# Performance work log

Measured on AMD Instinct MI355X. Metric: run time of the kernel, lower is better.

Reference implementation:

```python
import jax, jax.numpy as jnp
import numpy as np

B = 256          # graphs per batch
N_PER_G = 64     # nodes per graph
E_PER_G = 1024   # edges per graph
FN, FE, FG = 128, 128, 64
NA, HA, SO = 8, 256, 128


def _w(key, shape, scale=0.05):
    return jax.random.normal(key, shape, dtype=jnp.float32) * scale


def setup_inputs() -> dict:
    key = jax.random.key(0)
    ks = jax.random.split(key, 24)
    TN, TE = B * N_PER_G, B * E_PER_G
    inp = {
        'nodes': jax.random.normal(ks[0], (TN, FN), dtype=jnp.float32),
        'edges': jax.random.normal(ks[1], (TE, FE), dtype=jnp.float32),
        'globals_': jax.random.normal(ks[2], (B, FG), dtype=jnp.float32),
        'node_graph': jnp.repeat(jnp.arange(B, dtype=jnp.int32), N_PER_G),
        'edge_graph': jnp.repeat(jnp.arange(B, dtype=jnp.int32), E_PER_G),
        'a': jax.random.normal(ks[3], (B, NA), dtype=jnp.float32),
        # edge1: EdgeLinear(256, edge_features=FE)
        'We1': _w(ks[4], (FE, 256)), 'be1': jnp.zeros((256,), jnp.float32),
        # node1: NodeLinear(256, node_features=FN)
        'Wn1': _w(ks[5], (FN, 256)), 'bn1': jnp.zeros((256,), jnp.float32),
        # edge2: EdgeLinear(128, edge_features=256, global_features=FG)
        'We2_e': _w(ks[6], (256, 128)), 'We2_g': _w(ks[7], (FG, 128)), 'be2': jnp.zeros((128,), jnp.float32),
        # node2: NodeLinear(128, node_features=256, global_features=FG)
        'Wn2_n': _w(ks[8], (256, 128)), 'Wn2_g': _w(ks[9], (FG, 128)), 'bn2': jnp.zeros((128,), jnp.float32),
        # global: GlobalLinear(SO, node_features=128, edge_features=128, global_features=FG, aggregation='avg')
        'Wg_n': _w(ks[10], (128, SO)), 'Wg_e': _w(ks[11], (128, SO)), 'Wg_g': _w(ks[12], (FG, SO)), 'bg': jnp.zeros((SO,), jnp.float32),
        # action MLP
        'Wh': _w(ks[13], (SO + NA, HA)), 'bh': jnp.zeros((HA,), jnp.float32),
        'Wo': _w(ks[14], (HA, 1)), 'bo': jnp.zeros((1,), jnp.float32),
    }
    return inp


def _seg_mean(x, seg, num_segments):
    s = jax.ops.segment_sum(x, seg, num_segments=num_segments)
    c = jax.ops.segment_sum(jnp.ones((x.shape[0],), x.dtype), seg, num_segments=num_segments)
    return s / jnp.maximum(c, 1.0)[:, None]


def reference(nodes, edges, globals_, node_graph, edge_graph, a,
              We1, be1, Wn1, bn1, We2_e, We2_g, be2, Wn2_n, Wn2_g, bn2,
              Wg_n, Wg_e, Wg_g, bg, Wh, bh, Wo, bo):
    nb = globals_.shape[0]
    # edge1 + relu
    e = jax.nn.relu(edges @ We1 + be1)                                  # [TE,256]
    # node1 + relu
    n = jax.nn.relu(nodes @ Wn1 + bn1)                                  # [TN,256]
    # edge2 (edge feats + global broadcast to edges) + relu
    e = jax.nn.relu(e @ We2_e + globals_[edge_graph] @ We2_g + be2)     # [TE,128]
    # node2 (node feats + global broadcast to nodes) + relu
    n = jax.nn.relu(n @ Wn2_n + globals_[node_graph] @ Wn2_g + bn2)     # [TN,128]
    # global: avg-aggregate nodes and edges per graph + global linear
    n_avg = _seg_mean(n, node_graph, nb)                                # [B,128]
    e_avg = _seg_mean(e, edge_graph, nb)                                # [B,128]
    state_value = n_avg @ Wg_n + e_avg @ Wg_e + globals_ @ Wg_g + bg    # [B,SO]
    # action MLP
    sa = jnp.concatenate((state_value, a), axis=1)                      # [B,SO+NA]
    h = jax.nn.relu(sa @ Wh + bh)                                       # [B,HA]
    return h @ Wo + bo                                                  # [B,1]
```

## Files before the change

### kernel.cpp

```cpp
#include <hip/hip_runtime.h>

typedef unsigned short u16;
typedef __attribute__((ext_vector_type(8))) short s8v;
typedef __attribute__((ext_vector_type(4))) float f4v;

__device__ __forceinline__ float bf2f(u16 u) {
    union { unsigned int i; float f; } v;
    v.i = ((unsigned int)u) << 16;
    return v.f;
}
__device__ __forceinline__ u16 f2bf(float f) {
    union { float f; unsigned int i; } v;
    v.f = f;
    unsigned int x = v.i;
    x += 0x7FFFu + ((x >> 16) & 1u);
    return (u16)(x >> 16);
}
__device__ __forceinline__ float ldx(const void* p, long long i, int isf) {
    return isf ? ((const float*)p)[i] : bf2f(((const u16*)p)[i]);
}

__global__ void diag_kernel(const void* W, int* flag) {
    __shared__ int cnt;
    int t = threadIdx.x;
    if (t == 0) cnt = 0;
    __syncthreads();
    u16 u = ((const u16*)W)[2 * t];
    int e = (u >> 7) & 0xFF;
    int plausible = (e == 0) || (e >= 96 && e <= 140);
    atomicAdd(&cnt, plausible);
    __syncthreads();
    if (t == 0) *flag = (cnt < 128) ? 1 : 0;
}

__global__ void magic_kernel(void* out, float code) {
    ((u16*)out)[threadIdx.x] = f2bf(code);
}

__global__ void prep2_kernel(const void* We2_g, const void* Wn2_g,
                             const void* globals_,
                             const void* We1, const void* Wn1,
                             const void* We2_e, const void* Wn2_n,
                             const int* flag,
                             float* sums_zero, float* G2e, float* G2n,
                             u16* W1e_p, u16* W2e_p, u16* W1n_p, u16* W2n_p)
{
    int isf = *flag;
    int t = blockIdx.x * 256 + threadIdx.x;
    if (t < 65536) { sums_zero[t] = 0.f; return; }
    if (t < 131072) {
        int i = t - 65536;
        int which = i >> 15;
        int idx = i & 32767;
        int g = idx >> 7, c = idx & 127;
        const void* Wg = which ? Wn2_g : We2_g;
        float s = 0.f;
        for (int k = 0; k < 64; ++k)
            s += ldx(globals_, g * 64 + k, isf) * ldx(Wg, k * 128 + c, isf);
        if (which) G2n[idx] = s; else G2e[idx] = s;
        return;
    }
    int p = t - 131072;
    int which = p >> 12;
    int idx = p & 4095;
    int f = idx >> 6, lj = idx & 63;
    const void* W; u16* dst; int kb, nt, N;
    if (which == 0)      { W = We1;   dst = W1e_p; kb = f >> 4; nt = f & 15; N = 256; }
    else if (which == 1) { W = Wn1;   dst = W1n_p; kb = f >> 4; nt = f & 15; N = 256; }
    else if (which == 2) { W = We2_e; dst = W2e_p; kb = f >> 3; nt = f & 7;  N = 128; }
    else                 { W = Wn2_n; dst = W2n_p; kb = f >> 3; nt = f & 7;  N = 128; }
    int k0 = kb * 32 + 8 * (lj >> 4);
    int n  = nt * 16 + (lj & 15);
    s8v v;
#pragma unroll
    for (int j = 0; j < 8; ++j)
        v[j] = (short)f2bf(ldx(W, (long long)(k0 + j) * N + n, isf));
    *(s8v*)&dst[f * 512 + lj * 8] = v;
}

__global__ __launch_bounds__(256, 4) void QNetwork_89103391522965_kernel(
    const void* X, const void* b1, const void* b2,
    const u16* W1p, const u16* W2p, const float* gterm,
    const int* flag, float* sum_out, int rpg_shift)
{
    __shared__ u16 E1[64 * 256];
    const int isf  = *flag;
    const int tid  = threadIdx.x;
    const int lane = tid & 63;
    const int w    = tid >> 6;
    const int l15  = lane & 15;
    const int lg   = lane >> 4;
    const int m0   = blockIdx.x * 64;
    const int g    = m0 >> rpg_shift;

    f4v acc1[4][4];
#pragma unroll
    for (int nj = 0; nj < 4; ++nj) {
        float bv = ldx(b1, 64 * w + 16 * nj + l15, isf);
#pragma unroll
        for (int mi = 0; mi < 4; ++mi) {
            f4v t = {bv, bv, bv, bv};
            acc1[mi][nj] = t;
        }
    }

#pragma unroll
    for (int kb = 0; kb < 4; ++kb) {
        s8v a[4];
        const int k0 = kb * 32 + 8 * lg;
        if (!isf) {
#pragma unroll
            for (int mi = 0; mi < 4; ++mi)
                a[mi] = *(const s8v*)((const u16*)X +
                         (long long)(m0 + 16 * mi + l15) * 128 + k0);
        } else {
#pragma unroll
            for (int mi = 0; mi < 4; ++mi) {
                const float* xf = (const float*)X +
                         (long long)(m0 + 16 * mi + l15) * 128 + k0;
                s8v v;
#pragma unroll
                for (int j = 0; j < 8; ++j) v[j] = (short)f2bf(xf[j]);
                a[mi] = v;
            }
        }
#pragma unroll
        for (int nj = 0; nj < 4; ++nj) {
            s8v b = *(const s8v*)&W1p[(kb * 16 + 4 * w + nj) * 512 + lane * 8];
#pragma unroll
            for (int mi = 0; mi < 4; ++mi)
                acc1[mi][nj] = __builtin_amdgcn_mfma_f32_16x16x32_bf16(
                    a[mi], b, acc1[mi][nj], 0, 0, 0);
        }
    }

#pragma unroll
    for (int mi = 0; mi < 4; ++mi) {
#pragma unroll
        for (int nj = 0; nj < 4; ++nj) {
            int col = 64 * w + 16 * nj + l15;
#pragma unroll
            for (int r = 0; r < 4; ++r) {
                int row = 16 * mi + 4 * lg + r;
                int sw  = ((row ^ (row >> 1)) & 7) << 3;
                E1[(row * 256 + col) ^ sw] = f2bf(fmaxf(acc1[mi][nj][r], 0.f));
            }
        }
    }
    __syncthreads();

    f4v acc2[2][4];
#pragma unroll
    for (int mp = 0; mp < 2; ++mp)
#pragma unroll
        for (int nj = 0; nj < 4; ++nj) {
            f4v z = {0.f, 0.f, 0.f, 0.f};
            acc2[mp][nj] = z;
        }
    const int mbase = (w >> 1) * 2;
    const int nbase = (w & 1) * 4;

#pragma unroll
    for (int kb = 0; kb < 8; ++kb) {
        s8v a[2];
#pragma unroll
        for (int mp = 0; mp < 2; ++mp) {
            int row = (mbase + mp) * 16 + l15;
            int sw  = ((row ^ (row >> 1)) & 7) << 3;
            a[mp] = *(const s8v*)&E1[(row * 256 + kb * 32 + lg * 8) ^ sw];
        }
#pragma unroll
        for (int nj = 0; nj < 4; ++nj) {
            s8v b = *(const s8v*)&W2p[(kb * 8 + nbase + nj) * 512 + lane * 8];
#pragma unroll
            for (int mp = 0; mp < 2; ++mp)
                acc2[mp][nj] = __builtin_amdgcn_mfma_f32_16x16x32_bf16(
                    a[mp], b, acc2[mp][nj], 0, 0, 0);
        }
    }

#pragma unroll
    for (int nj = 0; nj < 4; ++nj) {
        int c2 = (nbase + nj) * 16 + l15;
        float add = gterm[g * 128 + c2] + ldx(b2, c2, isf);
        float s = 0.f;
#pragma unroll
        for (int mp = 0; mp < 2; ++mp)
#pragma unroll
            for (int r = 0; r < 4; ++r)
                s += fmaxf(acc2[mp][nj][r] + add, 0.f);
        s += __shfl_xor(s, 16);
        s += __shfl_xor(s, 32);
        if (lg == 0)
            atomicAdd(&sum_out[g * 128 + c2], s);
    }
}

__global__ void prep_kernel(const void* We2_g, const void* Wn2_g,
                            const void* globals_, const int* flag,
                            float* sums_zero, float* G2e, float* G2n)
{
    int isf = *flag;
    int t = blockIdx.x * 256 + threadIdx.x;
    if (t < 65536) {
        sums_zero[t] = 0.f;
    } else {
        int i = t - 65536;
        int which = i >> 15;
        int idx = i & 32767;
        int g = idx >> 7, c = idx & 127;
        const void* Wg = which ? Wn2_g : We2_g;
        float s = 0.f;
        for (int k = 0; k < 64; ++k)
            s += ldx(globals_, g * 64 + k, isf) * ldx(Wg, k * 128 + c, isf);
        if (which) G2n[idx] = s; else G2e[idx] = s;
    }
}

__global__ void QNetwork_89103391522965_valu(
    const void* X, const void* W1, const void* b1,
    const void* W2, const void* b2, const float* gterm,
    const int* flag, float* sum_out, int rows_per_graph)
{
    __shared__ u16 Xs[64 * 132];
    __shared__ u16 E1[64 * 260];
    __shared__ float accb[128];

    int isf = *flag;
    int tid = threadIdx.x;
    int m0 = blockIdx.x * 64;
    int g = m0 / rows_per_graph;

    if (tid < 128) accb[tid] = 0.f;

    for (int i = 0; i < 32; ++i) {
        int f = tid + i * 256;
        int row = f >> 7, col = f & 127;
        Xs[row * 132 + col] =
            f2bf(ldx(X, (long long)(m0 + row) * 128 + col, isf));
    }
    __syncthreads();

    {
        int c = tid;
        float binit = ldx(b1, c, isf);
        for (int rc = 0; rc < 4; ++rc) {
            float acc[16];
#pragma unroll
            for (int i = 0; i < 16; ++i) acc[i] = binit;
            for (int k = 0; k < 128; k += 2) {
                float w0 = ldx(W1, k * 256 + c, isf);
                float w1 = ldx(W1, (k + 1) * 256 + c, isf);
#pragma unroll
                for (int i = 0; i < 16; ++i) {
                    unsigned int xx =
                        *(const unsigned int*)&Xs[(rc * 16 + i) * 132 + k];
                    acc[i] += bf2f((u16)(xx & 0xFFFFu)) * w0;
                    acc[i] += bf2f((u16)(xx >> 16)) * w1;
                }
            }
#pragma unroll
            for (int i = 0; i < 16; ++i)
                E1[(rc * 16 + i) * 260 + c] = f2bf(fmaxf(acc[i], 0.f));
        }
    }
    __syncthreads();

    {
        int c2 = tid & 127;
        int rh = tid >> 7;
        float add = gterm[g * 128 + c2] + ldx(b2, c2, isf);
        float rowsum = 0.f;
        for (int rc = 0; rc < 2; ++rc) {
            int r0 = rh * 32 + rc * 16;
            float acc[16];
#pragma unroll
            for (int i = 0; i < 16; ++i) acc[i] = 0.f;
            for (int k = 0; k < 256; k += 2) {
                float w0 = ldx(W2, k * 128 + c2, isf);
                float w1 = ldx(W2, (k + 1) * 128 + c2, isf);
#pragma unroll
                for (int i = 0; i < 16; ++i) {
                    unsigned int xx =
                        *(const unsigned int*)&E1[(r0 + i) * 260 + k];
                    acc[i] += bf2f((u16)(xx & 0xFFFFu)) * w0;
                    acc[i] += bf2f((u16)(xx >> 16)) * w1;
                }
            }
#pragma unroll
            for (int i = 0; i < 16; ++i)
                rowsum += fmaxf(acc[i] + add, 0.f);
        }
        atomicAdd(&accb[c2], rowsum);
    }
    __syncthreads();
    if (tid < 128) atomicAdd(&sum_out[g * 128 + tid], accb[tid]);
}

__global__ void final_kernel(
    const float* e_sum, const float* n_sum,
    const void* globals_, const void* a_in,
    const void* Wg_n, const void* Wg_e, const void* Wg_g, const void* bg,
    const void* Wh, const void* bh, const void* Wo, const void* bo,
    const int* flag, void* out)
{
    __shared__ float navg[128], eavg[128], gv[64], sa[136];
    __shared__ float red[4];
    int isf = *flag;
    int g = blockIdx.x, t = threadIdx.x;

    if (t < 128) {
        navg[t] = n_sum[g * 128 + t] * (1.f / 64.f);
        eavg[t] = e_sum[g * 128 + t] * (1.f / 1024.f);
    } else if (t < 192) {
        gv[t - 128] = ldx(globals_, g * 64 + (t - 128), isf);
    }
    __syncthreads();

    if (t < 128) {
        float s = ldx(bg, t, isf);
        for (int k = 0; k < 128; ++k) s += navg[k] * ldx(Wg_n, k * 128 + t, isf);
        for (int k = 0; k < 128; ++k) s += eavg[k] * ldx(Wg_e, k * 128 + t, isf);
        for (int k = 0; k < 64;  ++k) s += gv[k]   * ldx(Wg_g, k * 128 + t, isf);
        sa[t] = s;
    } else if (t < 136) {
        sa[t] = ldx(a_in, g * 8 + (t - 128), isf);
    }
    __syncthreads();

    float s = ldx(bh, t, isf);
    for (int k = 0; k < 136; ++k) s += sa[k] * ldx(Wh, k * 256 + t, isf);
    float hv = fmaxf(s, 0.f) * ldx(Wo, t, isf);
#pragma unroll
    for (int off = 32; off; off >>= 1) hv += __shfl_down(hv, off);
    if ((t & 63) == 0) red[t >> 6] = hv;
    __syncthreads();
    if (t == 0) {
        float val = red[0] + red[1] + red[2] + red[3] + ldx(bo, 0, isf);
        if (isf) ((float*)out)[g] = val;
        else     ((u16*)out)[g]   = f2bf(val);
    }
}

extern "C" void kernel_launch(void* const* d_in, const int* in_sizes, int n_in,
                              void* d_out, int out_size, void* d_ws, size_t ws_size,
                              hipStream_t stream) {
    static const int EXPECT[24] = {
        2097152, 33554432, 16384, 16384, 262144, 2048,
        32768, 256, 32768, 256,
        32768, 8192, 128, 32768, 8192, 128,
        16384, 16384, 8192, 128,
        34816, 256, 256, 1
    };
    float code = 0.f;
    if (n_in != 24) code = 3000.f + n_in;
    else {
        for (int i = 0; i < 24; ++i)
            if (in_sizes[i] != EXPECT[i]) { code = 1000.f + i; break; }
    }
    if (ws_size < 524292 && code == 0.f) code = 4000.f;
    if (code != 0.f) {
        magic_kernel<<<1, 256, 0, stream>>>(d_out, code);
        return;
    }

    const void* nodes    = d_in[0];
    const void* edges    = d_in[1];
    const void* globals_ = d_in[2];
    const void* a_in  = d_in[5];
    const void* We1   = d_in[6];
    const void* be1   = d_in[7];
    const void* Wn1   = d_in[8];
    const void* bn1   = d_in[9];
    const void* We2_e = d_in[10];
    const void* We2_g = d_in[11];
    const void* be2   = d_in[12];
    const void* Wn2_n = d_in[13];
    const void* Wn2_g = d_in[14];
    const void* bn2   = d_in[15];
    const void* Wg_n  = d_in[16];
    const void* Wg_e  = d_in[17];
    const void* Wg_g  = d_in[18];
    const void* bg    = d_in[19];
    const void* Wh    = d_in[20];
    const void* bh    = d_in[21];
    const void* Wo    = d_in[22];
    const void* bo    = d_in[23];

    char* ws = (char*)d_ws;
    float* e_sum = (float*)(ws + 0);
    float* n_sum = (float*)(ws + 131072);
    float* G2e   = (float*)(ws + 262144);
    float* G2n   = (float*)(ws + 393216);

    if (ws_size >= 786436) {
        u16* W1e_p = (u16*)(ws + 524288);
        u16* W2e_p = (u16*)(ws + 589824);
        u16* W1n_p = (u16*)(ws + 655360);
        u16* W2n_p = (u16*)(ws + 720896);
        int* flag  = (int*)(ws + 786432);

        diag_kernel<<<1, 256, 0, stream>>>(We1, flag);
        prep2_kernel<<<576, 256, 0, stream>>>(We2_g, Wn2_g, globals_,
                                              We1, Wn1, We2_e, Wn2_n, flag,
                                              e_sum, G2e, G2n,
                                              W1e_p, W2e_p, W1n_p, W2n_p);
        QNetwork_89103391522965_kernel<<<4096, 256, 0, stream>>>(
            edges, be1, be2, W1e_p, W2e_p, G2e, flag, e_sum, 10);
        QNetwork_89103391522965_kernel<<<256, 256, 0, stream>>>(
            nodes, bn1, bn2, W1n_p, W2n_p, G2n, flag, n_sum, 6);
        final_kernel<<<256, 256, 0, stream>>>(e_sum, n_sum, globals_, a_in,
                                              Wg_n, Wg_e, Wg_g, bg, Wh, bh, Wo, bo,
                                              flag, d_out);
    } else {
        int* flag = (int*)(ws + 524288);
        diag_kernel<<<1, 256, 0, stream>>>(We1, flag);
        prep_kernel<<<512, 256, 0, stream>>>(We2_g, Wn2_g, globals_, flag,
                                             e_sum, G2e, G2n);
        QNetwork_89103391522965_valu<<<4096, 256, 0, stream>>>(
            edges, We1, be1, We2_e, be2, G2e, flag, e_sum, 1024);
        QNetwork_89103391522965_valu<<<256, 256, 0, stream>>>(
            nodes, Wn1, bn1, Wn2_n, bn2, G2n, flag, n_sum, 64);
        final_kernel<<<256, 256, 0, stream>>>(e_sum, n_sum, globals_, a_in,
                                              Wg_n, Wg_e, Wg_g, bg, Wh, bh, Wo, bo,
                                              flag, d_out);
    }
}
```

Measured before the change: 404.8 us.

## Merge edge and node MLP launches, process 256 rows per block with block-level reduction

Fuses the separate edge and node MLP kernels into one launch of 1088 blocks, where each block now loops over four 64-row tiles instead of one. Per-graph column sums are accumulated in registers and shared memory, so global atomics are issued once per graph per block rather than once per wave per tile. The diag kernel launch is dropped; each kernel infers the input dtype by sampling weight bits inline. Some scalar loops also get unroll pragmas. The costs are a longer serial loop per block, extra barriers, and redundant dtype probing in every block.

```diff
diff --git a/kernel.cpp b/kernel.cpp
--- a/kernel.cpp
+++ b/kernel.cpp
@@ -20,6 +20,18 @@
     return isf ? ((const float*)p)[i] : bf2f(((const u16*)p)[i]);
 }
 
+__device__ __forceinline__ int probe_isf(const void* W) {
+    const u16* p = (const u16*)W;
+    int cnt = 0;
+#pragma unroll
+    for (int i = 0; i < 32; ++i) {
+        u16 u = p[2 * i];
+        int e = (u >> 7) & 0xFF;
+        cnt += ((e == 0) || (e >= 96 && e <= 140)) ? 1 : 0;
+    }
+    return (cnt < 16) ? 1 : 0;
+}
+
 __global__ void diag_kernel(const void* W, int* flag) {
     __shared__ int cnt;
     int t = threadIdx.x;
@@ -41,11 +53,10 @@
                              const void* globals_,
                              const void* We1, const void* Wn1,
                              const void* We2_e, const void* Wn2_n,
-                             const int* flag,
                              float* sums_zero, float* G2e, float* G2n,
                              u16* W1e_p, u16* W2e_p, u16* W1n_p, u16* W2n_p)
 {
-    int isf = *flag;
+    int isf = probe_isf(We1);
     int t = blockIdx.x * 256 + threadIdx.x;
     if (t < 65536) { sums_zero[t] = 0.f; return; }
     if (t < 131072) {
@@ -55,6 +66,7 @@
         int g = idx >> 7, c = idx & 127;
         const void* Wg = which ? Wn2_g : We2_g;
         float s = 0.f;
+#pragma unroll 8
         for (int k = 0; k < 64; ++k)
             s += ldx(globals_, g * 64 + k, isf) * ldx(Wg, k * 128 + c, isf);
         if (which) G2n[idx] = s; else G2e[idx] = s;
@@ -79,120 +91,166 @@
 }
 
 __global__ __launch_bounds__(256, 4) void QNetwork_89103391522965_kernel(
-    const void* X, const void* b1, const void* b2,
-    const u16* W1p, const u16* W2p, const float* gterm,
-    const int* flag, float* sum_out, int rpg_shift)
+    const void* edges, const void* nodes,
+    const void* be1, const void* bn1, const void* be2, const void* bn2,
+    const u16* W1e, const u16* W2e, const u16* W1n, const u16* W2n,
+    const float* G2e, const float* G2n,
+    float* e_sum, float* n_sum, const void* probeW)
 {
     __shared__ u16 E1[64 * 256];
-    const int isf  = *flag;
+    __shared__ float accb[128];
+
+    const int isf  = probe_isf(probeW);
     const int tid  = threadIdx.x;
     const int lane = tid & 63;
     const int w    = tid >> 6;
     const int l15  = lane & 15;
     const int lg   = lane >> 4;
-    const int m0   = blockIdx.x * 64;
-    const int g    = m0 >> rpg_shift;
-
-    f4v acc1[4][4];
-#pragma unroll
-    for (int nj = 0; nj < 4; ++nj) {
-        float bv = ldx(b1, 64 * w + 16 * nj + l15, isf);
-#pragma unroll
-        for (int mi = 0; mi < 4; ++mi) {
-            f4v t = {bv, bv, bv, bv};
-            acc1[mi][nj] = t;
-        }
-    }
-
-#pragma unroll
-    for (int kb = 0; kb < 4; ++kb) {
-        s8v a[4];
-        const int k0 = kb * 32 + 8 * lg;
-        if (!isf) {
-#pragma unroll
-            for (int mi = 0; mi < 4; ++mi)
-                a[mi] = *(const s8v*)((const u16*)X +
-                         (long long)(m0 + 16 * mi + l15) * 128 + k0);
-        } else {
-#pragma unroll
-            for (int mi = 0; mi < 4; ++mi) {
-                const float* xf = (const float*)X +
-                         (long long)(m0 + 16 * mi + l15) * 128 + k0;
-                s8v v;
-#pragma unroll
-                for (int j = 0; j < 8; ++j) v[j] = (short)f2bf(xf[j]);
-                a[mi] = v;
-            }
-        }
+
+    const int bid = blockIdx.x;
+    const bool isn = bid >= 1024;
+    const int rb = isn ? (bid - 1024) : bid;
+    const void* X   = isn ? nodes : edges;
+    const void* b1  = isn ? bn1 : be1;
+    const void* b2  = isn ? bn2 : be2;
+    const u16* W1p  = isn ? W1n : W1e;
+    const u16* W2p  = isn ? W2n : W2e;
+    const float* gt = isn ? G2n : G2e;
+    float* sum      = isn ? n_sum : e_sum;
+    const int rpgs  = isn ? 6 : 10;
+    const int rowbase = rb * 256;
+
+    if (tid < 128) accb[tid] = 0.f;
+
+    const int nbase = (w & 1) * 4;
+    const int mb16  = (w >> 1) * 32;
+
+    float binit[4];
+#pragma unroll
+    for (int nj = 0; nj < 4; ++nj)
+        binit[nj] = ldx(b1, 64 * w + 16 * nj + l15, isf);
+
+    float rs[4] = {0.f, 0.f, 0.f, 0.f};
+    float add[4];
+
+    for (int t = 0; t < 4; ++t) {
+        const int m0 = rowbase + t * 64;
+        const int g  = m0 >> rpgs;
+        if (t == 0 || rpgs == 6) {
+#pragma unroll
+            for (int nj = 0; nj < 4; ++nj) {
+                int c2 = (nbase + nj) * 16 + l15;
+                add[nj] = gt[g * 128 + c2] + ldx(b2, c2, isf);
+            }
+        }
+
+#pragma unroll
+        for (int mh = 0; mh < 2; ++mh) {
+            f4v acc1[2][4];
+#pragma unroll
+            for (int nj = 0; nj < 4; ++nj) {
+                f4v tv = {binit[nj], binit[nj], binit[nj], binit[nj]};
+                acc1[0][nj] = tv; acc1[1][nj] = tv;
+            }
+#pragma unroll
+            for (int kb = 0; kb < 4; ++kb) {
+                s8v a[2];
+                const int k0 = kb * 32 + 8 * lg;
+#pragma unroll
+                for (int mi = 0; mi < 2; ++mi) {
+                    const int row = m0 + (mh * 2 + mi) * 16 + l15;
+                    if (!isf) {
+                        a[mi] = *(const s8v*)((const u16*)X +
+                                 (long long)row * 128 + k0);
+                    } else {
+                        const float* xf = (const float*)X +
+                                 (long long)row * 128 + k0;
+                        s8v v;
+#pragma unroll
+                        for (int j = 0; j < 8; ++j) v[j] = (short)f2bf(xf[j]);
+                        a[mi] = v;
+                    }
+                }
+#pragma unroll
+                for (int nj = 0; nj < 4; ++nj) {
+                    s8v b = *(const s8v*)&W1p[(kb * 16 + 4 * w + nj) * 512 + lane * 8];
+#pragma unroll
+                    for (int mi = 0; mi < 2; ++mi)
+                        acc1[mi][nj] = __builtin_amdgcn_mfma_f32_16x16x32_bf16(
+                            a[mi], b, acc1[mi][nj], 0, 0, 0);
+                }
+            }
+#pragma unroll
+            for (int mi = 0; mi < 2; ++mi)
+#pragma unroll
+                for (int nj = 0; nj < 4; ++nj) {
+                    int col = 64 * w + 16 * nj + l15;
+#pragma unroll
+                    for (int r = 0; r < 4; ++r) {
+                        int row = (mh * 2 + mi) * 16 + 4 * lg + r;
+                        int sw  = ((row ^ (row >> 1)) & 7) << 3;
+                        E1[(row * 256 + col) ^ sw] = f2bf(fmaxf(acc1[mi][nj][r], 0.f));
+                    }
+                }
+        }
+        __syncthreads();
+
+        f4v acc2[2][4];
+#pragma unroll
+        for (int mp = 0; mp < 2; ++mp)
+#pragma unroll
+            for (int nj = 0; nj < 4; ++nj) {
+                f4v z = {0.f, 0.f, 0.f, 0.f};
+                acc2[mp][nj] = z;
+            }
+#pragma unroll
+        for (int kb = 0; kb < 8; ++kb) {
+            s8v a2[2];
+#pragma unroll
+            for (int mp = 0; mp < 2; ++mp) {
+                int row = mb16 + mp * 16 + l15;
+                int sw  = ((row ^ (row >> 1)) & 7) << 3;
+                a2[mp] = *(const s8v*)&E1[(row * 256 + kb * 32 + lg * 8) ^ sw];
+            }
+#pragma unroll
+            for (int nj = 0; nj < 4; ++nj) {
+                s8v b = *(const s8v*)&W2p[(kb * 8 + nbase + nj) * 512 + lane * 8];
+#pragma unroll
+                for (int mp = 0; mp < 2; ++mp)
+                    acc2[mp][nj] = __builtin_amdgcn_mfma_f32_16x16x32_bf16(
+                        a2[mp], b, acc2[mp][nj], 0, 0, 0);
+            }
+        }
+
 #pragma unroll
         for (int nj = 0; nj < 4; ++nj) {
-            s8v b = *(const s8v*)&W1p[(kb * 16 + 4 * w + nj) * 512 + lane * 8];
-#pragma unroll
-            for (int mi = 0; mi < 4; ++mi)
-                acc1[mi][nj] = __builtin_amdgcn_mfma_f32_16x16x32_bf16(
-                    a[mi], b, acc1[mi][nj], 0, 0, 0);
-        }
-    }
-
-#pragma unroll
-    for (int mi = 0; mi < 4; ++mi) {
-#pragma unroll
-        for (int nj = 0; nj < 4; ++nj) {
-            int col = 64 * w + 16 * nj + l15;
-#pragma unroll
-            for (int r = 0; r < 4; ++r) {
-                int row = 16 * mi + 4 * lg + r;
-                int sw  = ((row ^ (row >> 1)) & 7) << 3;
-                E1[(row * 256 + col) ^ sw] = f2bf(fmaxf(acc1[mi][nj][r], 0.f));
-            }
-        }
-    }
-    __syncthreads();
-
-    f4v acc2[2][4];
-#pragma unroll
-    for (int mp = 0; mp < 2; ++mp)
-#pragma unroll
-        for (int nj = 0; nj < 4; ++nj) {
-            f4v z = {0.f, 0.f, 0.f, 0.f};
-            acc2[mp][nj] = z;
-        }
-    const int mbase = (w >> 1) * 2;
-    const int nbase = (w & 1) * 4;
-
-#pragma unroll
-    for (int kb = 0; kb < 8; ++kb) {
-        s8v a[2];
-#pragma unroll
-        for (int mp = 0; mp < 2; ++mp) {
-            int row = (mbase + mp) * 16 + l15;
-            int sw  = ((row ^ (row >> 1)) & 7) << 3;
-            a[mp] = *(const s8v*)&E1[(row * 256 + kb * 32 + lg * 8) ^ sw];
-        }
-#pragma unroll
-        for (int nj = 0; nj < 4; ++nj) {
-            s8v b = *(const s8v*)&W2p[(kb * 8 + nbase + nj) * 512 + lane * 8];
+            float s = 0.f;
 #pragma unroll
             for (int mp = 0; mp < 2; ++mp)
-                acc2[mp][nj] = __builtin_amdgcn_mfma_f32_16x16x32_bf16(
-                    a[mp], b, acc2[mp][nj], 0, 0, 0);
-        }
-    }
-
-#pragma unroll
-    for (int nj = 0; nj < 4; ++nj) {
-        int c2 = (nbase + nj) * 16 + l15;
-        float add = gterm[g * 128 + c2] + ldx(b2, c2, isf);
-        float s = 0.f;
-#pragma unroll
-        for (int mp = 0; mp < 2; ++mp)
-#pragma unroll
-            for (int r = 0; r < 4; ++r)
-                s += fmaxf(acc2[mp][nj][r] + add, 0.f);
-        s += __shfl_xor(s, 16);
-        s += __shfl_xor(s, 32);
-        if (lg == 0)
-            atomicAdd(&sum_out[g * 128 + c2], s);
+#pragma unroll
+                for (int r = 0; r < 4; ++r)
+                    s += fmaxf(acc2[mp][nj][r] + add[nj], 0.f);
+            rs[nj] += s;
+        }
+
+        const bool fl = (t == 3) || (rpgs == 6);
+        if (fl) {
+#pragma unroll
+            for (int nj = 0; nj < 4; ++nj) {
+                float v = rs[nj];
+                v += __shfl_xor(v, 16);
+                v += __shfl_xor(v, 32);
+                if (lg == 0)
+                    atomicAdd(&accb[(nbase + nj) * 16 + l15], v);
+                rs[nj] = 0.f;
+            }
+            __syncthreads();
+            if (tid < 128) {
+                atomicAdd(&sum[g * 128 + tid], accb[tid]);
+                accb[tid] = 0.f;
+            }
+        }
+        __syncthreads();
     }
 }
 
@@ -302,11 +360,11 @@
     const void* globals_, const void* a_in,
     const void* Wg_n, const void* Wg_e, const void* Wg_g, const void* bg,
     const void* Wh, const void* bh, const void* Wo, const void* bo,
-    const int* flag, void* out)
+    const void* probeW, void* out)
 {
     __shared__ float navg[128], eavg[128], gv[64], sa[136];
     __shared__ float red[4];
-    int isf = *flag;
+    int isf = probe_isf(probeW);
     int g = blockIdx.x, t = threadIdx.x;
 
     if (t < 128) {
@@ -319,8 +377,11 @@
 
     if (t < 128) {
         float s = ldx(bg, t, isf);
+#pragma unroll 8
         for (int k = 0; k < 128; ++k) s += navg[k] * ldx(Wg_n, k * 128 + t, isf);
+#pragma unroll 8
         for (int k = 0; k < 128; ++k) s += eavg[k] * ldx(Wg_e, k * 128 + t, isf);
+#pragma unroll 8
         for (int k = 0; k < 64;  ++k) s += gv[k]   * ldx(Wg_g, k * 128 + t, isf);
         sa[t] = s;
     } else if (t < 136) {
@@ -329,6 +390,7 @@
     __syncthreads();
 
     float s = ldx(bh, t, isf);
+#pragma unroll 8
     for (int k = 0; k < 136; ++k) s += sa[k] * ldx(Wh, k * 256 + t, isf);
     float hv = fmaxf(s, 0.f) * ldx(Wo, t, isf);
 #pragma unroll
@@ -398,20 +460,18 @@
         u16* W2e_p = (u16*)(ws + 589824);
         u16* W1n_p = (u16*)(ws + 655360);
         u16* W2n_p = (u16*)(ws + 720896);
-        int* flag  = (int*)(ws + 786432);
-
-        diag_kernel<<<1, 256, 0, stream>>>(We1, flag);
+
         prep2_kernel<<<576, 256, 0, stream>>>(We2_g, Wn2_g, globals_,
-                                              We1, Wn1, We2_e, Wn2_n, flag,
+                                              We1, Wn1, We2_e, Wn2_n,
                                               e_sum, G2e, G2n,
                                               W1e_p, W2e_p, W1n_p, W2n_p);
-        QNetwork_89103391522965_kernel<<<4096, 256, 0, stream>>>(
-            edges, be1, be2, W1e_p, W2e_p, G2e, flag, e_sum, 10);
-        QNetwork_89103391522965_kernel<<<256, 256, 0, stream>>>(
-            nodes, bn1, bn2, W1n_p, W2n_p, G2n, flag, n_sum, 6);
+        QNetwork_89103391522965_kernel<<<1088, 256, 0, stream>>>(
+            edges, nodes, be1, bn1, be2, bn2,
+            W1e_p, W2e_p, W1n_p, W2n_p, G2e, G2n,
+            e_sum, n_sum, We1);
         final_kernel<<<256, 256, 0, stream>>>(e_sum, n_sum, globals_, a_in,
                                               Wg_n, Wg_e, Wg_g, bg, Wh, bh, Wo, bo,
-                                              flag, d_out);
+                                              We1, d_out);
     } else {
         int* flag = (int*)(ws + 524288);
         diag_kernel<<<1, 256, 0, stream>>>(We1, flag);
@@ -423,6 +483,6 @@
             nodes, Wn1, bn1, Wn2_n, bn2, G2n, flag, n_sum, 64);
         final_kernel<<<256, 256, 0, stream>>>(e_sum, n_sum, globals_, a_in,
                                               Wg_n, Wg_e, Wg_g, bg, Wh, bh, Wo, bo,
-                                              flag, d_out);
-    }
-}
+                                              We1, d_out);
+    }
+}
```

After: 643.2 us. 1.59x slower.
